# Performance work log

Hardware: AMD Instinct MI355X
Metric: run time of the kernel (lower is better)

## Reference

```python
import jax, jax.numpy as jnp
import numpy as np

IN_CH = 256
QK_CH = IN_CH // 8  # 32

def setup_inputs() -> dict:
    key = jax.random.key(0)
    ks = jax.random.split(key, 7)
    x = jax.random.normal(ks[0], (4, IN_CH, 64, 64), dtype=jnp.float32)
    s_in = 1.0 / np.sqrt(IN_CH)
    # 1x1 conv weights stored as [out_ch, in_ch]; biases [out_ch]
    Wq = jax.random.uniform(ks[1], (QK_CH, IN_CH), jnp.float32, -s_in, s_in)
    bq = jax.random.uniform(ks[2], (QK_CH,), jnp.float32, -s_in, s_in)
    Wk = jax.random.uniform(ks[3], (QK_CH, IN_CH), jnp.float32, -s_in, s_in)
    bk = jax.random.uniform(ks[4], (QK_CH,), jnp.float32, -s_in, s_in)
    Wv = jax.random.uniform(ks[5], (IN_CH, IN_CH), jnp.float32, -s_in, s_in)
    bv = jax.random.uniform(ks[6], (IN_CH,), jnp.float32, -s_in, s_in)
    return {"x": x, "Wq": Wq, "bq": bq, "Wk": Wk, "bk": bk, "Wv": Wv, "bv": bv}

def reference(x, Wq, bq, Wk, bk, Wv, bv):
    n, c, h, w = x.shape
    xf = x.reshape(n, c, h * w)  # [n, c, hw]
    # 1x1 convs == per-position channel matmuls
    q = jnp.einsum('oc,ncs->nos', Wq, xf) + bq[None, :, None]  # [n, c/8, hw]
    k = jnp.einsum('oc,ncs->nos', Wk, xf) + bk[None, :, None]  # [n, c/8, hw]
    v = jnp.einsum('oc,ncs->nos', Wv, xf) + bv[None, :, None]  # [n, c,  hw]
    # energy[n, i, j] = <q[:, i], k[:, j]>  (no scaling, as in original)
    energy = jnp.einsum('nci,ncj->nij', q, k)  # [n, hw, hw]
    attention = jax.nn.softmax(energy, axis=-1)
    # out[n, c, i] = sum_j v[n, c, j] * attention[n, i, j]
    out = jnp.einsum('ncj,nij->nci', v, attention)
    return out.reshape(n, c, h, w)
```

## Files before the change

### kernel.cpp

```cpp
#include <hip/hip_runtime.h>
#include <hip/hip_bf16.h>
#include <stdint.h>
#include <stddef.h>

typedef unsigned short u16;
typedef unsigned int   u32;
typedef __attribute__((ext_vector_type(8))) short bf16x8;
typedef __attribute__((ext_vector_type(4))) float f32x4;

#define LOG2E   1.44269504f
#define EXP_OFF 23.0831206f

static __device__ __forceinline__ float bf2f(u16 v) {
    u32 u = ((u32)v) << 16; float f; __builtin_memcpy(&f, &u, 4); return f;
}
static __device__ __forceinline__ u16 f2bf(float f) {
    u32 u; __builtin_memcpy(&u, &f, 4);
    u32 r = (u + 0x7fffu + ((u >> 16) & 1u)) >> 16; return (u16)r;
}
static __device__ __forceinline__ float as_f(u32 u) { float f; __builtin_memcpy(&f, &u, 4); return f; }
static __device__ __forceinline__ u32   as_u(float f) { u32 u; __builtin_memcpy(&u, &f, 4); return u; }

static __device__ __forceinline__ int detect_f32_wave0(const void* x, int t) {
    const u32* xw = (const u32*)x;
    int bad = 0;
    #pragma unroll
    for (int k = 0; k < 4; ++k) {
        u32 wv = xw[(t << 2) + k];
        int e = (wv >> 7) & 0xff;
        bad += (e >= 160);
    }
    unsigned long long m = __ballot(bad > 0);
    return (__popcll(m) >= 8) ? 1 : 0;
}

__global__ __launch_bounds__(256) void qkv_proj_kernel(
    const void* __restrict__ x,
    const void* __restrict__ Wq, const void* __restrict__ bq,
    const void* __restrict__ Wk, const void* __restrict__ bk,
    const void* __restrict__ Wv, const void* __restrict__ bv,
    u16* __restrict__ qws, u16* __restrict__ kws, u16* __restrict__ vws,
    int n_off)
{
    __shared__ float Ws[32][68];
    __shared__ float Xs[32][68];
    __shared__ int dtf;

    const int t   = threadIdx.x;
    const int it  = blockIdx.x;
    const int ot  = blockIdx.y;
    const int n_w = blockIdx.z;
    const int n_g = n_off + n_w;
    const int i0  = it << 6;
    const int tx  = t & 15;
    const int ty  = t >> 4;

    if (t < 64) { int f = detect_f32_wave0(x, t); if (t == 0) dtf = f; }
    __syncthreads();
    const bool isf32 = (dtf != 0);

    float acc[4][4];
    #pragma unroll
    for (int a = 0; a < 4; ++a)
        #pragma unroll
        for (int b = 0; b < 4; ++b) acc[a][b] = 0.f;

    const int o_st   = t & 63;
    const int kk0    = (t >> 6) << 3;
    const int och_st = (ot << 6) + o_st;
    int wsel, wrow;
    if (och_st < 32)      { wsel = 0; wrow = och_st; }
    else if (och_st < 64) { wsel = 1; wrow = och_st - 32; }
    else                  { wsel = 2; wrow = och_st - 64; }
    const void* wbase = (wsel == 0) ? Wq : (wsel == 1) ? Wk : Wv;

    for (int c0 = 0; c0 < 256; c0 += 32) {
        if (isf32) {
            const float* wf = (const float*)wbase + wrow * 256 + c0 + kk0;
            #pragma unroll
            for (int k8 = 0; k8 < 8; ++k8) Ws[kk0 + k8][o_st] = wf[k8];
            const float* xf = (const float*)x;
            #pragma unroll
            for (int v = 0; v < 2; ++v) {
                int g  = t + (v << 8);
                int kk = g >> 4;
                int ii = (g & 15) << 2;
                float4 x4 = *(const float4*)(xf +
                    (((size_t)(n_g * 256 + c0 + kk)) << 12) + i0 + ii);
                Xs[kk][ii + 0] = x4.x; Xs[kk][ii + 1] = x4.y;
                Xs[kk][ii + 2] = x4.z; Xs[kk][ii + 3] = x4.w;
            }
        } else {
            const u16* wh = (const u16*)wbase + wrow * 256 + c0 + kk0;
            #pragma unroll
            for (int k8 = 0; k8 < 8; ++k8) Ws[kk0 + k8][o_st] = bf2f(wh[k8]);
            const u16* xh = (const u16*)x;
            #pragma unroll
            for (int v = 0; v < 2; ++v) {
                int g  = t + (v << 8);
                int kk = g >> 4;
                int ii = (g & 15) << 2;
                ushort4 u4 = *(const ushort4*)(xh +
                    (((size_t)(n_g * 256 + c0 + kk)) << 12) + i0 + ii);
                Xs[kk][ii + 0] = bf2f(u4.x); Xs[kk][ii + 1] = bf2f(u4.y);
                Xs[kk][ii + 2] = bf2f(u4.z); Xs[kk][ii + 3] = bf2f(u4.w);
            }
        }
        __syncthreads();

        #pragma unroll
        for (int kk = 0; kk < 32; ++kk) {
            float4 a4 = *(const float4*)&Ws[kk][ty << 2];
            float4 b4 = *(const float4*)&Xs[kk][tx << 2];
            float av[4] = {a4.x, a4.y, a4.z, a4.w};
            float bw[4] = {b4.x, b4.y, b4.z, b4.w};
            #pragma unroll
            for (int a = 0; a < 4; ++a)
                #pragma unroll
                for (int b = 0; b < 4; ++b)
                    acc[a][b] += av[a] * bw[b];
        }
        __syncthreads();
    }

    #pragma unroll
    for (int a = 0; a < 4; ++a) {
        int och = (ot << 6) + (ty << 2) + a;
        float bias;
        if (isf32) {
            if (och < 32)      bias = ((const float*)bq)[och];
            else if (och < 64) bias = ((const float*)bk)[och - 32];
            else               bias = ((const float*)bv)[och - 64];
        } else {
            if (och < 32)      bias = bf2f(((const u16*)bq)[och]);
            else if (och < 64) bias = bf2f(((const u16*)bk)[och - 32]);
            else               bias = bf2f(((const u16*)bv)[och - 64]);
        }
        if (och < 32) {
            #pragma unroll
            for (int b = 0; b < 4; ++b) {
                int i = i0 + (tx << 2) + b;
                qws[(((size_t)(n_w << 12) + i) << 5) + och] =
                    f2bf((acc[a][b] + bias) * LOG2E);
            }
        } else if (och < 64) {
            #pragma unroll
            for (int b = 0; b < 4; ++b) {
                int i = i0 + (tx << 2) + b;
                kws[(((size_t)(n_w << 12) + i) << 5) + (och - 32)] =
                    f2bf(acc[a][b] + bias);
            }
        } else {
            ushort4 h;
            h.x = f2bf(acc[a][0] + bias);
            h.y = f2bf(acc[a][1] + bias);
            h.z = f2bf(acc[a][2] + bias);
            h.w = f2bf(acc[a][3] + bias);
            *(ushort4*)(vws + (((size_t)n_w) << 20)
                        + ((size_t)(och - 64) << 12) + i0 + (tx << 2)) = h;
        }
    }
}

__global__ __launch_bounds__(1024) void flash_mfma4(
    const u16* __restrict__ qws, const u16* __restrict__ kws,
    const u16* __restrict__ vws, void* __restrict__ out,
    const void* __restrict__ x, int n_off, int nshift)
{
    __shared__ __align__(16) char arena[81920];
    __shared__ __align__(16) float lS[64];
    __shared__ int dtf;
    u16*   VsA  = (u16*)arena;
    u16*   PsA  = (u16*)(arena + 65536);
    float* Dbuf = (float*)arena;

    const int t    = threadIdx.x;
    const int lane = t & 63;
    const int w    = t >> 6;
    const int n16  = lane & 15;
    const int quad = lane >> 4;
    const int bid  = blockIdx.x;
    const int n_w  = bid & ((1 << nshift) - 1);
    const int qt   = bid >> nshift;
    const int n_g  = n_off + n_w;
    const int i0   = qt << 6;

    if (t < 64) {
        int f = detect_f32_wave0(x, t);
        if (t == 0) dtf = f;
        lS[t] = 0.f;
    }

    const u16* qb = qws + (((size_t)n_w) << 17);
    const u16* kb = kws + (((size_t)n_w) << 17);
    const u16* vb = vws + (((size_t)n_w) << 20);

    const int qsub_s = w & 3;
    const int jsub   = w >> 2;
    const int qh = w & 1;
    const int cq = (w >> 1) & 3;
    const int jq = w >> 3;

    const bf16x8 qfrag =
        *(const bf16x8*)(qb + ((size_t)(i0 + (qsub_s << 4) + n16) << 5) + (quad << 3));

    f32x4 acc[2][4];
    #pragma unroll
    for (int a = 0; a < 2; ++a)
        #pragma unroll
        for (int b = 0; b < 4; ++b) acc[a][b] = (f32x4){0.f, 0.f, 0.f, 0.f};
    float lp[4] = {0.f, 0.f, 0.f, 0.f};

    const int vc  = t >> 3;
    const int vg  = t & 7;
    const int vsw = (vg ^ (vc & 7)) << 3;

    const int jcol = (jsub << 4) + n16;
    const int j8   = jcol >> 3;
    const int jlo  = jcol & 7;
    const int ksw  = (jq << 2) + quad;

    uint4 vreg0, vreg1;
    bf16x8 kreg;

    vreg0 = *(const uint4*)(vb + (size_t)vc * 4096 + (vg << 3));
    vreg1 = *(const uint4*)(vb + (size_t)(vc + 128) * 4096 + (vg << 3));
    kreg  = *(const bf16x8*)(kb + ((size_t)((jsub << 4) + n16) << 5) + (quad << 3));
    {
        u16* Vs = VsA;
        u16* Ps = PsA;
        *(uint4*)&Vs[vc * 64 + vsw]         = vreg0;
        *(uint4*)&Vs[(vc + 128) * 64 + vsw] = vreg1;
        const f32x4 z = {0.f, 0.f, 0.f, 0.f};
        f32x4 s = __builtin_amdgcn_mfma_f32_16x16x32_bf16(qfrag, kreg, z, 0, 0, 0);
        #pragma unroll
        for (int r = 0; r < 4; ++r) {
            const int qrow = (qsub_s << 4) + (quad << 2) + r;
            float p = exp2f(s[r] - EXP_OFF);
            u32 u = as_u(p) & 0xffff0000u;
            lp[r] += as_f(u);
            Ps[qrow * 64 + ((j8 ^ (qrow & 7)) << 3) + jlo] = (u16)(u >> 16);
        }
        vreg0 = *(const uint4*)(vb + (size_t)vc * 4096 + 64 + (vg << 3));
        vreg1 = *(const uint4*)(vb + (size_t)(vc + 128) * 4096 + 64 + (vg << 3));
        kreg  = *(const bf16x8*)(kb + ((size_t)(64 + (jsub << 4) + n16) << 5) + (quad << 3));
    }
    __syncthreads();

    for (int tile = 1; tile < 64; ++tile) {
        const int par  = tile & 1;
        const int parp = par ^ 1;
        u16* Vsc = VsA + (par  << 14);
        u16* Psc = PsA + (par  << 12);
        u16* Vsp = VsA + (parp << 14);
        u16* Psp = PsA + (parp << 12);

        bf16x8 pa[2];
        #pragma unroll
        for (int qs = 0; qs < 2; ++qs) {
            const int qrow = (qh << 5) + (qs << 4) + n16;
            pa[qs] = *(const bf16x8*)&Psp[qrow * 64 + ((ksw ^ (qrow & 7)) << 3)];
        }
        #pragma unroll
        for (int cs = 0; cs < 4; ++cs) {
            const int crow = (cq << 6) + (cs << 4) + n16;
            bf16x8 vf = *(const bf16x8*)&Vsp[crow * 64 + ((ksw ^ (crow & 7)) << 3)];
            #pragma unroll
            for (int qs = 0; qs < 2; ++qs)
                acc[qs][cs] = __builtin_amdgcn_mfma_f32_16x16x32_bf16(
                    pa[qs], vf, acc[qs][cs], 0, 0, 0);
        }

        *(uint4*)&Vsc[vc * 64 + vsw]         = vreg0;
        *(uint4*)&Vsc[(vc + 128) * 64 + vsw] = vreg1;

        const f32x4 z = {0.f, 0.f, 0.f, 0.f};
        f32x4 s = __builtin_amdgcn_mfma_f32_16x16x32_bf16(qfrag, kreg, z, 0, 0, 0);
        #pragma unroll
        for (int r = 0; r < 4; ++r) {
            const int qrow = (qsub_s << 4) + (quad << 2) + r;
            float p = exp2f(s[r] - EXP_OFF);
            u32 u = as_u(p) & 0xffff0000u;
            lp[r] += as_f(u);
            Psc[qrow * 64 + ((j8 ^ (qrow & 7)) << 3) + jlo] = (u16)(u >> 16);
        }

        if (tile < 63) {
            const int j0n = (tile + 1) << 6;
            vreg0 = *(const uint4*)(vb + (size_t)vc * 4096 + j0n + (vg << 3));
            vreg1 = *(const uint4*)(vb + (size_t)(vc + 128) * 4096 + j0n + (vg << 3));
            kreg  = *(const bf16x8*)(kb + ((size_t)(j0n + (jsub << 4) + n16) << 5)
                                     + (quad << 3));
        }
        __syncthreads();
    }

    {
        u16* Vsp = VsA + (1 << 14);
        u16* Psp = PsA + (1 << 12);
        bf16x8 pa[2];
        #pragma unroll
        for (int qs = 0; qs < 2; ++qs) {
            const int qrow = (qh << 5) + (qs << 4) + n16;
            pa[qs] = *(const bf16x8*)&Psp[qrow * 64 + ((ksw ^ (qrow & 7)) << 3)];
        }
        #pragma unroll
        for (int cs = 0; cs < 4; ++cs) {
            const int crow = (cq << 6) + (cs << 4) + n16;
            bf16x8 vf = *(const bf16x8*)&Vsp[crow * 64 + ((ksw ^ (crow & 7)) << 3)];
            #pragma unroll
            for (int qs = 0; qs < 2; ++qs)
                acc[qs][cs] = __builtin_amdgcn_mfma_f32_16x16x32_bf16(
                    pa[qs], vf, acc[qs][cs], 0, 0, 0);
        }
    }

    #pragma unroll
    for (int r = 0; r < 4; ++r) {
        lp[r] += __shfl_xor(lp[r], 1);
        lp[r] += __shfl_xor(lp[r], 2);
        lp[r] += __shfl_xor(lp[r], 4);
        lp[r] += __shfl_xor(lp[r], 8);
    }
    if (n16 == 0) {
        #pragma unroll
        for (int r = 0; r < 4; ++r)
            atomicAdd(&lS[(qsub_s << 4) + (quad << 2) + r], lp[r]);
    }
    __syncthreads();
    if (t < 64) lS[t] = 1.0f / lS[t];
    const bool isf32 = (dtf != 0);

    for (int chunk = 0; chunk < 4; ++chunk) {
        __syncthreads();
        if (jq == 1 && cq == chunk) {
            #pragma unroll
            for (int qs = 0; qs < 2; ++qs)
                #pragma unroll
                for (int cs = 0; cs < 4; ++cs)
                    *(f32x4*)&Dbuf[((cs << 4) + n16) * 68 +
                                   (qh << 5) + (qs << 4) + (quad << 2)] = acc[qs][cs];
        }
        __syncthreads();
        if (jq == 0 && cq == chunk) {
            #pragma unroll
            for (int qs = 0; qs < 2; ++qs)
                #pragma unroll
                for (int cs = 0; cs < 4; ++cs) {
                    float* p = &Dbuf[((cs << 4) + n16) * 68 +
                                     (qh << 5) + (qs << 4) + (quad << 2)];
                    f32x4 d = *(f32x4*)p;
                    d += acc[qs][cs];
                    *(f32x4*)p = d;
                }
        }
        __syncthreads();
        const int c_l = t >> 4;
        const int qg  = (t & 15) << 2;
        float4 d  = *(float4*)&Dbuf[c_l * 68 + qg];
        float4 rl = *(float4*)&lS[qg];
        const int c_glob = (chunk << 6) + c_l;
        const size_t ob = (((size_t)(n_g * 256 + c_glob)) << 12) + i0 + qg;
        if (isf32) {
            float4 o = make_float4(d.x * rl.x, d.y * rl.y, d.z * rl.z, d.w * rl.w);
            *(float4*)((float*)out + ob) = o;
        } else {
            union { uint2 v; u16 h[4]; } o;
            o.h[0] = f2bf(d.x * rl.x);
            o.h[1] = f2bf(d.y * rl.y);
            o.h[2] = f2bf(d.z * rl.z);
            o.h[3] = f2bf(d.w * rl.w);
            *(uint2*)((u16*)out + ob) = o.v;
        }
    }
}

extern "C" void kernel_launch(void* const* d_in, const int* in_sizes, int n_in,
                              void* d_out, int out_size, void* d_ws, size_t ws_size,
                              hipStream_t stream)
{
    const void* x  = d_in[0];
    const void* Wq = d_in[1];
    const void* bq = d_in[2];
    const void* Wk = d_in[3];
    const void* bk = d_in[4];
    const void* Wv = d_in[5];
    const void* bv = d_in[6];

    const size_t full_need = (size_t)(4u * 4096u) * (32 + 32 + 256) * 2;
    if (ws_size >= full_need) {
        u16* qws = (u16*)d_ws;
        u16* kws = qws + (size_t)4 * 4096 * 32;
        u16* vws = kws + (size_t)4 * 4096 * 32;
        qkv_proj_kernel<<<dim3(64, 5, 4), dim3(256), 0, stream>>>(
            x, Wq, bq, Wk, bk, Wv, bv, qws, kws, vws, 0);
        flash_mfma4<<<dim3(256), dim3(1024), 0, stream>>>(
            qws, kws, vws, d_out, x, 0, 2);
    } else {
        u16* qws = (u16*)d_ws;
        u16* kws = qws + (size_t)4096 * 32;
        u16* vws = kws + (size_t)4096 * 32;
        for (int n = 0; n < 4; ++n) {
            qkv_proj_kernel<<<dim3(64, 5, 1), dim3(256), 0, stream>>>(
                x, Wq, bq, Wk, bk, Wv, bv, qws, kws, vws, n);
            flash_mfma4<<<dim3(64), dim3(1024), 0, stream>>>(
                qws, kws, vws, d_out, x, n, 0);
        }
    }
}
```

Measured before the change: 169.0 us.

## Load V fragments directly from global into registers, dropping V LDS staging

The V tile is no longer staged through shared memory. Each wave now reads its MFMA B-operand fragments straight from global memory into registers, one tile ahead. The wave-to-work mapping changes so each wave owns 32 channels across all 64 query rows (4x2 accumulators instead of 2x4). Shared memory drops from about 80KB to about 18KB, which removes the LDS write and read traffic for V and could allow more occupancy. The cost is more redundant global and L2 reads of V, because fragments are shared across waves only through cache, and the global latency is hidden by just one tile of prefetch.

```diff
diff --git a/kernel.cpp b/kernel.cpp
--- a/kernel.cpp
+++ b/kernel.cpp
@@ -162,16 +162,15 @@
     }
 }
 
-__global__ __launch_bounds__(1024) void flash_mfma4(
+__global__ __launch_bounds__(1024) void flash_mfma5(
     const u16* __restrict__ qws, const u16* __restrict__ kws,
     const u16* __restrict__ vws, void* __restrict__ out,
     const void* __restrict__ x, int n_off, int nshift)
 {
-    __shared__ __align__(16) char arena[81920];
+    __shared__ __align__(16) char arena[17920];
     __shared__ __align__(16) float lS[64];
     __shared__ int dtf;
-    u16*   VsA  = (u16*)arena;
-    u16*   PsA  = (u16*)(arena + 65536);
+    u16*   PsA  = (u16*)arena;
     float* Dbuf = (float*)arena;
 
     const int t    = threadIdx.x;
@@ -197,40 +196,32 @@
 
     const int qsub_s = w & 3;
     const int jsub   = w >> 2;
-    const int qh = w & 1;
-    const int cq = (w >> 1) & 3;
+    const int cq = w & 7;
     const int jq = w >> 3;
 
     const bf16x8 qfrag =
         *(const bf16x8*)(qb + ((size_t)(i0 + (qsub_s << 4) + n16) << 5) + (quad << 3));
 
-    f32x4 acc[2][4];
-    #pragma unroll
-    for (int a = 0; a < 2; ++a)
-        #pragma unroll
-        for (int b = 0; b < 4; ++b) acc[a][b] = (f32x4){0.f, 0.f, 0.f, 0.f};
+    f32x4 acc[4][2];
+    #pragma unroll
+    for (int a = 0; a < 4; ++a)
+        #pragma unroll
+        for (int b = 0; b < 2; ++b) acc[a][b] = (f32x4){0.f, 0.f, 0.f, 0.f};
     float lp[4] = {0.f, 0.f, 0.f, 0.f};
-
-    const int vc  = t >> 3;
-    const int vg  = t & 7;
-    const int vsw = (vg ^ (vc & 7)) << 3;
 
     const int jcol = (jsub << 4) + n16;
     const int j8   = jcol >> 3;
     const int jlo  = jcol & 7;
     const int ksw  = (jq << 2) + quad;
 
-    uint4 vreg0, vreg1;
-    bf16x8 kreg;
-
-    vreg0 = *(const uint4*)(vb + (size_t)vc * 4096 + (vg << 3));
-    vreg1 = *(const uint4*)(vb + (size_t)(vc + 128) * 4096 + (vg << 3));
-    kreg  = *(const bf16x8*)(kb + ((size_t)((jsub << 4) + n16) << 5) + (quad << 3));
+    const u16* vfp0 = vb + (size_t)((cq << 5) + n16) * 4096 + (jq << 5) + (quad << 3);
+    const u16* vfp1 = vfp0 + (size_t)16 * 4096;
+
+    bf16x8 kreg, vf0, vf1;
+
+    kreg = *(const bf16x8*)(kb + ((size_t)((jsub << 4) + n16) << 5) + (quad << 3));
     {
-        u16* Vs = VsA;
         u16* Ps = PsA;
-        *(uint4*)&Vs[vc * 64 + vsw]         = vreg0;
-        *(uint4*)&Vs[(vc + 128) * 64 + vsw] = vreg1;
         const f32x4 z = {0.f, 0.f, 0.f, 0.f};
         f32x4 s = __builtin_amdgcn_mfma_f32_16x16x32_bf16(qfrag, kreg, z, 0, 0, 0);
         #pragma unroll
@@ -241,38 +232,31 @@
             lp[r] += as_f(u);
             Ps[qrow * 64 + ((j8 ^ (qrow & 7)) << 3) + jlo] = (u16)(u >> 16);
         }
-        vreg0 = *(const uint4*)(vb + (size_t)vc * 4096 + 64 + (vg << 3));
-        vreg1 = *(const uint4*)(vb + (size_t)(vc + 128) * 4096 + 64 + (vg << 3));
-        kreg  = *(const bf16x8*)(kb + ((size_t)(64 + (jsub << 4) + n16) << 5) + (quad << 3));
+        kreg = *(const bf16x8*)(kb + ((size_t)(64 + (jsub << 4) + n16) << 5) + (quad << 3));
+        vf0 = *(const bf16x8*)(vfp0);
+        vf1 = *(const bf16x8*)(vfp1);
     }
     __syncthreads();
 
     for (int tile = 1; tile < 64; ++tile) {
         const int par  = tile & 1;
-        const int parp = par ^ 1;
-        u16* Vsc = VsA + (par  << 14);
-        u16* Psc = PsA + (par  << 12);
-        u16* Vsp = VsA + (parp << 14);
-        u16* Psp = PsA + (parp << 12);
-
-        bf16x8 pa[2];
-        #pragma unroll
-        for (int qs = 0; qs < 2; ++qs) {
-            const int qrow = (qh << 5) + (qs << 4) + n16;
+        u16* Psc = PsA + (par << 12);
+        u16* Psp = PsA + ((par ^ 1) << 12);
+
+        bf16x8 pa[4];
+        #pragma unroll
+        for (int qs = 0; qs < 4; ++qs) {
+            const int qrow = (qs << 4) + n16;
             pa[qs] = *(const bf16x8*)&Psp[qrow * 64 + ((ksw ^ (qrow & 7)) << 3)];
         }
         #pragma unroll
-        for (int cs = 0; cs < 4; ++cs) {
-            const int crow = (cq << 6) + (cs << 4) + n16;
-            bf16x8 vf = *(const bf16x8*)&Vsp[crow * 64 + ((ksw ^ (crow & 7)) << 3)];
-            #pragma unroll
-            for (int qs = 0; qs < 2; ++qs)
-                acc[qs][cs] = __builtin_amdgcn_mfma_f32_16x16x32_bf16(
-                    pa[qs], vf, acc[qs][cs], 0, 0, 0);
-        }
-
-        *(uint4*)&Vsc[vc * 64 + vsw]         = vreg0;
-        *(uint4*)&Vsc[(vc + 128) * 64 + vsw] = vreg1;
+        for (int qs = 0; qs < 4; ++qs) {
+            acc[qs][0] = __builtin_amdgcn_mfma_f32_16x16x32_bf16(pa[qs], vf0, acc[qs][0], 0, 0, 0);
+            acc[qs][1] = __builtin_amdgcn_mfma_f32_16x16x32_bf16(pa[qs], vf1, acc[qs][1], 0, 0, 0);
+        }
+
+        vf0 = *(const bf16x8*)(vfp0 + (tile << 6));
+        vf1 = *(const bf16x8*)(vfp1 + (tile << 6));
 
         const f32x4 z = {0.f, 0.f, 0.f, 0.f};
         f32x4 s = __builtin_amdgcn_mfma_f32_16x16x32_bf16(qfrag, kreg, z, 0, 0, 0);
@@ -287,31 +271,24 @@
 
         if (tile < 63) {
             const int j0n = (tile + 1) << 6;
-            vreg0 = *(const uint4*)(vb + (size_t)vc * 4096 + j0n + (vg << 3));
-            vreg1 = *(const uint4*)(vb + (size_t)(vc + 128) * 4096 + j0n + (vg << 3));
-            kreg  = *(const bf16x8*)(kb + ((size_t)(j0n + (jsub << 4) + n16) << 5)
-                                     + (quad << 3));
+            kreg = *(const bf16x8*)(kb + ((size_t)(j0n + (jsub << 4) + n16) << 5)
+                                    + (quad << 3));
         }
         __syncthreads();
     }
 
     {
-        u16* Vsp = VsA + (1 << 14);
         u16* Psp = PsA + (1 << 12);
-        bf16x8 pa[2];
-        #pragma unroll
-        for (int qs = 0; qs < 2; ++qs) {
-            const int qrow = (qh << 5) + (qs << 4) + n16;
+        bf16x8 pa[4];
+        #pragma unroll
+        for (int qs = 0; qs < 4; ++qs) {
+            const int qrow = (qs << 4) + n16;
             pa[qs] = *(const bf16x8*)&Psp[qrow * 64 + ((ksw ^ (qrow & 7)) << 3)];
         }
         #pragma unroll
-        for (int cs = 0; cs < 4; ++cs) {
-            const int crow = (cq << 6) + (cs << 4) + n16;
-            bf16x8 vf = *(const bf16x8*)&Vsp[crow * 64 + ((ksw ^ (crow & 7)) << 3)];
-            #pragma unroll
-            for (int qs = 0; qs < 2; ++qs)
-                acc[qs][cs] = __builtin_amdgcn_mfma_f32_16x16x32_bf16(
-                    pa[qs], vf, acc[qs][cs], 0, 0, 0);
+        for (int qs = 0; qs < 4; ++qs) {
+            acc[qs][0] = __builtin_amdgcn_mfma_f32_16x16x32_bf16(pa[qs], vf0, acc[qs][0], 0, 0, 0);
+            acc[qs][1] = __builtin_amdgcn_mfma_f32_16x16x32_bf16(pa[qs], vf1, acc[qs][1], 0, 0, 0);
         }
     }
 
@@ -333,22 +310,22 @@
 
     for (int chunk = 0; chunk < 4; ++chunk) {
         __syncthreads();
-        if (jq == 1 && cq == chunk) {
-            #pragma unroll
-            for (int qs = 0; qs < 2; ++qs)
+        if (jq == 1 && (cq >> 1) == chunk) {
+            #pragma unroll
+            for (int qs = 0; qs < 4; ++qs)
                 #pragma unroll
-                for (int cs = 0; cs < 4; ++cs)
-                    *(f32x4*)&Dbuf[((cs << 4) + n16) * 68 +
-                                   (qh << 5) + (qs << 4) + (quad << 2)] = acc[qs][cs];
-        }
-        __syncthreads();
-        if (jq == 0 && cq == chunk) {
-            #pragma unroll
-            for (int qs = 0; qs < 2; ++qs)
+                for (int cs = 0; cs < 2; ++cs)
+                    *(f32x4*)&Dbuf[(((cq & 1) << 5) + (cs << 4) + n16) * 68 +
+                                   (qs << 4) + (quad << 2)] = acc[qs][cs];
+        }
+        __syncthreads();
+        if (jq == 0 && (cq >> 1) == chunk) {
+            #pragma unroll
+            for (int qs = 0; qs < 4; ++qs)
                 #pragma unroll
-                for (int cs = 0; cs < 4; ++cs) {
-                    float* p = &Dbuf[((cs << 4) + n16) * 68 +
-                                     (qh << 5) + (qs << 4) + (quad << 2)];
+                for (int cs = 0; cs < 2; ++cs) {
+                    float* p = &Dbuf[(((cq & 1) << 5) + (cs << 4) + n16) * 68 +
+                                     (qs << 4) + (quad << 2)];
                     f32x4 d = *(f32x4*)p;
                     d += acc[qs][cs];
                     *(f32x4*)p = d;
@@ -394,7 +371,7 @@
         u16* vws = kws + (size_t)4 * 4096 * 32;
         qkv_proj_kernel<<<dim3(64, 5, 4), dim3(256), 0, stream>>>(
             x, Wq, bq, Wk, bk, Wv, bv, qws, kws, vws, 0);
-        flash_mfma4<<<dim3(256), dim3(1024), 0, stream>>>(
+        flash_mfma5<<<dim3(256), dim3(1024), 0, stream>>>(
             qws, kws, vws, d_out, x, 0, 2);
     } else {
         u16* qws = (u16*)d_ws;
@@ -403,7 +380,7 @@
         for (int n = 0; n < 4; ++n) {
             qkv_proj_kernel<<<dim3(64, 5, 1), dim3(256), 0, stream>>>(
                 x, Wq, bq, Wk, bk, Wv, bv, qws, kws, vws, n);
-            flash_mfma4<<<dim3(64), dim3(1024), 0, stream>>>(
+            flash_mfma5<<<dim3(64), dim3(1024), 0, stream>>>(
                 qws, kws, vws, d_out, x, n, 0);
         }
     }
```

New measurement: 197.2 us. 16.7% more time.
